# Kernel optimization log

Measured on AMD Instinct MI355X. Metric: run time of the kernel, lower is better.

The kernel has to match this reference:

```python
import jax, jax.numpy as jnp
import numpy as np

D_MODEL = 1024
D_K = 1024
D_V = 1024
N_HEAD = 16
EPS = 1e-5
BS, N_TOK = 2, 2048


def setup_inputs() -> dict:
    key = jax.random.key(0)
    ks = jax.random.split(key, 12)
    s = 0.02
    q = jax.random.normal(ks[0], (BS, N_TOK, D_MODEL), jnp.float32)
    k = jax.random.normal(ks[1], (BS, N_TOK, D_MODEL), jnp.float32)
    v = jax.random.normal(ks[2], (BS, N_TOK, D_MODEL), jnp.float32)
    return {
        "q": q, "k": k, "v": v,
        "gamma": jnp.ones((D_MODEL,), jnp.float32),
        "beta": jnp.zeros((D_MODEL,), jnp.float32),
        "Wq": jax.random.normal(ks[3], (D_MODEL, D_K), jnp.float32) * s,
        "bq": jnp.zeros((D_K,), jnp.float32),
        "Wk": jax.random.normal(ks[4], (D_MODEL, D_K), jnp.float32) * s,
        "bk": jnp.zeros((D_K,), jnp.float32),
        "Wv": jax.random.normal(ks[5], (D_MODEL, D_V), jnp.float32) * s,
        "bv": jnp.zeros((D_V,), jnp.float32),
        "Wo": jax.random.normal(ks[6], (D_V, D_MODEL), jnp.float32) * s,
        "bo": jnp.zeros((D_MODEL,), jnp.float32),
    }


def reference(q, k, v, gamma, beta, Wq, bq, Wk, bk, Wv, bv, Wo, bo):
    # NOTE: original module ignores k, v args; self-attention over q.
    bs, n_tok, d_m = q.shape
    d_h = D_K // N_HEAD
    temper = float(np.sqrt(d_h))

    # LayerNorm1d over d_model
    mu = jnp.mean(q, axis=-1, keepdims=True)
    var = jnp.var(q, axis=-1, keepdims=True)
    h = (q - mu) / jnp.sqrt(var + EPS) * gamma + beta

    # projections; head split = chunk along feature dim -> [bs, H, T, d_h]
    qh = (h @ Wq + bq).reshape(bs, n_tok, N_HEAD, d_h).transpose(0, 2, 1, 3)
    kh = (h @ Wk + bk).reshape(bs, n_tok, N_HEAD, d_h).transpose(0, 2, 1, 3)
    vh = jax.nn.relu(h @ Wv + bv).reshape(bs, n_tok, N_HEAD, d_h).transpose(0, 2, 1, 3)

    scores = jnp.einsum('bhqd,bhkd->bhqk', qh, kh) / temper
    # dropout before softmax in train mode; identity in eval (deterministic ref)
    attn = jax.nn.softmax(scores, axis=-1)
    o = jnp.einsum('bhqk,bhkd->bhqd', attn, vh)  # [bs, H, T, d_h]

    # faithful to torch: view(bs, n_tok, -1) with NO head transpose (head-major merge)
    merged = o.reshape(bs, n_tok, N_HEAD * d_h)
    out = merged @ Wo + bo + q  # proj + residual
    return out
```

## Files before the change

### kernel.cpp

```cpp
#include <hip/hip_runtime.h>

typedef __bf16 bf16;
typedef __bf16 bf16x8 __attribute__((ext_vector_type(8)));
typedef __bf16 bf16x4 __attribute__((ext_vector_type(4)));
typedef float  f32x4  __attribute__((ext_vector_type(4)));
typedef float  f32x16 __attribute__((ext_vector_type(16)));
typedef unsigned int u32;
typedef u32 u32x4 __attribute__((ext_vector_type(4)));

#define AS1U(p) ((const __attribute__((address_space(1))) unsigned int*)(p))
#define AS3U(p) ((__attribute__((address_space(3))) unsigned int*)(p))

static __device__ __forceinline__ u32 pack2(float a, float b) {
    unsigned short ua = __builtin_bit_cast(unsigned short, (bf16)a);
    unsigned short ub = __builtin_bit_cast(unsigned short, (bf16)b);
    return (u32)ua | ((u32)ub << 16);
}

__global__ void transpose_cast4_kernel(const float* __restrict__ W0, const float* __restrict__ W1,
                                       const float* __restrict__ W2, const float* __restrict__ W3,
                                       bf16* __restrict__ D0, bf16* __restrict__ D1,
                                       bf16* __restrict__ D2, bf16* __restrict__ D3) {
    __shared__ float tile[32][33];
    const float* W; bf16* D;
    switch (blockIdx.z) {
        case 0: W = W0; D = D0; break;
        case 1: W = W1; D = D1; break;
        case 2: W = W2; D = D2; break;
        default: W = W3; D = D3; break;
    }
    const int bj = blockIdx.x, bi = blockIdx.y;
    const int tx = threadIdx.x, ty = threadIdx.y;
#pragma unroll
    for (int i = 0; i < 4; i++) {
        tile[ty + i * 8][tx] = W[(size_t)(bi * 32 + ty + i * 8) * 1024 + bj * 32 + tx];
    }
    __syncthreads();
#pragma unroll
    for (int i = 0; i < 4; i++) {
        D[(size_t)(bj * 32 + ty + i * 8) * 1024 + bi * 32 + tx] =
            (bf16)tile[tx][ty + i * 8];
    }
}

__global__ void layernorm_kernel(const float* __restrict__ x,
                                 const float* __restrict__ gamma,
                                 const float* __restrict__ beta,
                                 bf16* __restrict__ h) {
    const int row = blockIdx.x;
    const float* xr = x + (size_t)row * 1024;
    const int t = threadIdx.x;
    float4 v = ((const float4*)xr)[t];
    float s  = v.x + v.y + v.z + v.w;
    float s2 = v.x * v.x + v.y * v.y + v.z * v.z + v.w * v.w;
#pragma unroll
    for (int m = 1; m < 64; m <<= 1) {
        s  += __shfl_xor(s, m, 64);
        s2 += __shfl_xor(s2, m, 64);
    }
    __shared__ float ssum[4], ssum2[4];
    const int wid = t >> 6, lane = t & 63;
    if (lane == 0) { ssum[wid] = s; ssum2[wid] = s2; }
    __syncthreads();
    s  = ssum[0] + ssum[1] + ssum[2] + ssum[3];
    s2 = ssum2[0] + ssum2[1] + ssum2[2] + ssum2[3];
    const float mu  = s * (1.f / 1024.f);
    const float var = s2 * (1.f / 1024.f) - mu * mu;
    const float rs  = rsqrtf(var + 1e-5f);
    float4 g = ((const float4*)gamma)[t];
    float4 b = ((const float4*)beta)[t];
    bf16x4 o;
    o[0] = (bf16)((v.x - mu) * rs * g.x + b.x);
    o[1] = (bf16)((v.y - mu) * rs * g.y + b.y);
    o[2] = (bf16)((v.z - mu) * rs * g.z + b.z);
    o[3] = (bf16)((v.w - mu) * rs * g.w + b.w);
    ((bf16x4*)(h + (size_t)row * 1024))[t] = o;
}

template <int EPI>
__global__ void gemm_kernel(const bf16* __restrict__ A, const bf16* __restrict__ BT,
                            int N, int K,
                            bf16* __restrict__ Cb,
                            const float* __restrict__ b0, const float* __restrict__ b1,
                            const float* __restrict__ b2, bf16* __restrict__ Vt,
                            float* __restrict__ Cf, const float* __restrict__ bo,
                            const float* __restrict__ resid) {
    __shared__ bf16 Asm[128][32];
    __shared__ bf16 Bsm[128][32];
    const int tid = threadIdx.x;
    const int lane = tid & 63, wave = tid >> 6;
    const int wr = wave >> 1, wc = wave & 1;
    const int nwg = gridDim.x * gridDim.y;
    const int bid0 = blockIdx.y * gridDim.x + blockIdx.x;
    const int bid = (bid0 & 7) * (nwg >> 3) + (bid0 >> 3);
    const int tileN = (bid % gridDim.x) * 128;
    const int tileM = (bid / gridDim.x) * 128;
    const int row16 = lane & 15, g = lane >> 4;

    f32x4 acc[4][4] = {};

    for (int kt = 0; kt < K; kt += 32) {
#pragma unroll
        for (int i = 0; i < 2; i++) {
            int c = tid + i * 256;
            int r = c >> 2, cb = (c & 3) * 16;
            const char* g_ = (const char*)(A + (size_t)(tileM + r) * K + kt) + cb;
            char* l_ = (char*)&Asm[0][0] + c * 16;
            __builtin_amdgcn_global_load_lds(AS1U(g_), AS3U(l_), 16, 0, 0);
        }
#pragma unroll
        for (int i = 0; i < 2; i++) {
            int c = tid + i * 256;
            int r = c >> 2, cb = (c & 3) * 16;
            const char* g_ = (const char*)(BT + (size_t)(tileN + r) * K + kt) + cb;
            char* l_ = (char*)&Bsm[0][0] + c * 16;
            __builtin_amdgcn_global_load_lds(AS1U(g_), AS3U(l_), 16, 0, 0);
        }
        __syncthreads();
        bf16x8 af[4], bfr[4];
#pragma unroll
        for (int m = 0; m < 4; m++)
            af[m] = *(const bf16x8*)&Asm[wr * 64 + m * 16 + row16][g * 8];
#pragma unroll
        for (int n = 0; n < 4; n++)
            bfr[n] = *(const bf16x8*)&Bsm[wc * 64 + n * 16 + row16][g * 8];
#pragma unroll
        for (int m = 0; m < 4; m++)
#pragma unroll
            for (int n = 0; n < 4; n++)
                acc[m][n] = __builtin_amdgcn_mfma_f32_16x16x32_bf16(af[m], bfr[n],
                                                                   acc[m][n], 0, 0, 0);
        __syncthreads();
    }

    if constexpr (EPI == 0) {
        __shared__ bf16 Ep[4][64][64];
        char* ep = (char*)&Ep[wave][0][0];
        const bool isV = (tileN >= 2048);
        if (!isV) {
#pragma unroll
            for (int n = 0; n < 4; n++) {
                const int cl = n * 16 + row16;
                const int gc = tileN + wc * 64 + cl;
                const float bias = gc < 1024 ? b0[gc] : b1[gc - 1024];
                const float scl = gc < 1024 ? 0.18033688011112042f : 1.f;
#pragma unroll
                for (int m = 0; m < 4; m++)
#pragma unroll
                    for (int j = 0; j < 4; j++) {
                        const int rl = m * 16 + g * 4 + j;
                        const float v = (acc[m][n][j] + bias) * scl;
                        *(bf16*)(ep + rl * 128 + ((cl * 2) ^ ((rl & 7) << 4))) = (bf16)v;
                    }
            }
        } else {
#pragma unroll
            for (int n = 0; n < 4; n++) {
                const int dl = n * 16 + row16;
                const float bias = b2[(tileN - 2048) + wc * 64 + dl];
#pragma unroll
                for (int m = 0; m < 4; m++)
#pragma unroll
                    for (int j = 0; j < 4; j++) {
                        const int tl = m * 16 + g * 4 + j;
                        const float v = fmaxf(acc[m][n][j] + bias, 0.f);
                        *(bf16*)(ep + dl * 128 + ((tl * 2) ^ ((dl & 7) << 4))) = (bf16)v;
                    }
            }
        }
        asm volatile("s_waitcnt lgkmcnt(0)" ::: "memory");
        __builtin_amdgcn_sched_barrier(0);
        if (!isV) {
#pragma unroll
            for (int it = 0; it < 8; it++) {
                const int rl = (lane >> 3) + it * 8;
                const bf16x8 vrow = *(const bf16x8*)(ep + rl * 128 +
                                                     (((lane & 7) * 16) ^ ((rl & 7) << 4)));
                const int gr = tileM + wr * 64 + rl;
                const int gc = tileN + wc * 64 + (lane & 7) * 8;
                *(bf16x8*)&Cb[(size_t)gr * N + gc] = vrow;
            }
        } else {
            const int bb = tileM >> 11;
            const int tbase = (tileM & 2047) + wr * 64 + (lane & 7) * 8;
#pragma unroll
            for (int it = 0; it < 8; it++) {
                const int dl = (lane >> 3) + it * 8;
                const bf16x8 vrow = *(const bf16x8*)(ep + dl * 128 +
                                                     (((lane & 7) * 16) ^ ((dl & 7) << 4)));
                const int gd = (tileN - 2048) + wc * 64 + dl;
                const int hh = gd >> 6, dd = gd & 63;
                *(bf16x8*)&Vt[(((size_t)bb * 16 + hh) * 64 + dd) * 2048 + tbase] = vrow;
            }
        }
    } else {
#pragma unroll
        for (int m = 0; m < 4; m++) {
            const int row = tileM + wr * 64 + m * 16 + g * 4;
#pragma unroll
            for (int n = 0; n < 4; n++) {
                const int col = tileN + wc * 64 + n * 16 + row16;
#pragma unroll
                for (int j = 0; j < 4; j++) {
                    const int r = row + j;
                    Cf[(size_t)r * N + col] = acc[m][n][j] + bo[col] +
                                              resid[(size_t)r * N + col];
                }
            }
        }
    }
}

__global__ __launch_bounds__(512, 4)
void attn_kernel(const bf16* __restrict__ qkv, const bf16* __restrict__ Vt,
                 bf16* __restrict__ Obuf) {
    const int bid = blockIdx.x;
    const int swz = (bid & 7) * 64 + (bid >> 3);
    const int bh = swz >> 4, qt = swz & 15;
    const int b = bh >> 4, h = bh & 15;
    const int qbase = qt * 128;
    const int tid = threadIdx.x;
    const int lane = tid & 63, wv = tid >> 6;
    const int half = wv >> 2, qw = wv & 3;
    const int c = lane & 31, p = lane >> 5;

    __shared__ bf16 Kl[2][2][64][64];
    __shared__ bf16 Vl[2][2][64][64];

    const bf16* qrow = qkv + (size_t)(b * 2048 + qbase + qw * 32 + c) * 3072 + h * 64;
    bf16x8 qf[4];
#pragma unroll
    for (int ch = 0; ch < 4; ch++)
        qf[ch] = *(const bf16x8*)(qrow + ch * 16 + p * 8);

    const char* kgbase = (const char*)(qkv + (size_t)b * 2048 * 3072 + 1024 + h * 64)
                         + (size_t)(half * 1024) * 6144;
    const char* vgbase = (const char*)(Vt + (size_t)bh * 64 * 2048) + half * 2048;
    const int ht = tid & 255;
    const char* kgp[2]; const char* vgp[2]; int ldo[2];
#pragma unroll
    for (int i = 0; i < 2; i++) {
        const int cc = ht + i * 256;
        const int srow = cc >> 3;
        const int scol = ((cc & 7) * 16) ^ ((srow & 7) << 4);
        kgp[i] = kgbase + (size_t)srow * 6144 + scol;
        vgp[i] = vgbase + (size_t)srow * 4096 + scol;
        ldo[i] = cc * 16;
    }
    char* kldb = (char*)&Kl[half][0][0][0];
    char* vldb = (char*)&Vl[half][0][0][0];

    auto stage = [&](int t, int slot) {
        const size_t ko = (size_t)t * (64 * 6144);
        const size_t vo = (size_t)t * 128;
        const int sb = slot * 8192;
#pragma unroll
        for (int i = 0; i < 2; i++) {
            __builtin_amdgcn_global_load_lds(AS1U(kgp[i] + ko), AS3U(kldb + sb + ldo[i]), 16, 0, 0);
            __builtin_amdgcn_global_load_lds(AS1U(vgp[i] + vo), AS3U(vldb + sb + ldo[i]), 16, 0, 0);
        }
    };

    f32x16 accO[2] = {};
    float l_r = 0.f;

    auto compute = [&](int slot) {
        const char* Kb = (const char*)&Kl[half][slot][0][0];
        const char* Vb = (const char*)&Vl[half][slot][0][0];
#pragma unroll
        for (int cc = 0; cc < 2; cc++) {
            f32x16 accT = {};
            const int tok = cc * 32 + c;
#pragma unroll
            for (int ch = 0; ch < 4; ch++) {
                const bf16x8 kf = *(const bf16x8*)(Kb + tok * 128 +
                                                   ((ch * 32 + p * 16) ^ ((tok & 7) << 4)));
                accT = __builtin_amdgcn_mfma_f32_32x32x16_bf16(kf, qf[ch], accT, 0, 0, 0);
            }
            float pv[16];
#pragma unroll
            for (int r = 0; r < 16; r++) pv[r] = exp2f(accT[r]);
            float s01 = (pv[0] + pv[1]) + (pv[2] + pv[3]);
            float s23 = (pv[4] + pv[5]) + (pv[6] + pv[7]);
            float s45 = (pv[8] + pv[9]) + (pv[10] + pv[11]);
            float s67 = (pv[12] + pv[13]) + (pv[14] + pv[15]);
            l_r += (s01 + s23) + (s45 + s67);
            u32 k01 = pack2(pv[0], pv[1]),  k23 = pack2(pv[2], pv[3]);
            u32 k45 = pack2(pv[4], pv[5]),  k67 = pack2(pv[6], pv[7]);
            u32 k89 = pack2(pv[8], pv[9]),  kab = pack2(pv[10], pv[11]);
            u32 kcd = pack2(pv[12], pv[13]), kef = pack2(pv[14], pv[15]);
            asm("v_permlane32_swap_b32 %0, %1" : "+v"(k45), "+v"(k01));
            asm("v_permlane32_swap_b32 %0, %1" : "+v"(k67), "+v"(k23));
            asm("v_permlane32_swap_b32 %0, %1" : "+v"(kcd), "+v"(k89));
            asm("v_permlane32_swap_b32 %0, %1" : "+v"(kef), "+v"(kab));
            u32x4 w0w = {k01, k23, k45, k67};
            u32x4 w1w = {k89, kab, kcd, kef};
            const bf16x8 pf0 = __builtin_bit_cast(bf16x8, w0w);
            const bf16x8 pf1 = __builtin_bit_cast(bf16x8, w1w);
#pragma unroll
            for (int dc = 0; dc < 2; dc++) {
                const int rd = dc * 32 + c;
                const int sw = (rd & 7) << 4;
                const bf16x8 vf0 = *(const bf16x8*)(Vb + rd * 128 + ((cc * 64 + p * 16) ^ sw));
                const bf16x8 vf1 = *(const bf16x8*)(Vb + rd * 128 + ((cc * 64 + 32 + p * 16) ^ sw));
                accO[dc] = __builtin_amdgcn_mfma_f32_32x32x16_bf16(pf0, vf0, accO[dc], 0, 0, 0);
                accO[dc] = __builtin_amdgcn_mfma_f32_32x32x16_bf16(pf1, vf1, accO[dc], 0, 0, 0);
            }
        }
    };

#define KV_SYNC() do { \
        asm volatile("s_waitcnt vmcnt(0)" ::: "memory"); \
        __builtin_amdgcn_s_barrier(); \
        asm volatile("" ::: "memory"); \
    } while (0)

    stage(0, 0);
#pragma unroll 1
    for (int t = 0; t < 14; t += 2) {
        KV_SYNC(); stage(t + 1, 1); compute(0);
        KV_SYNC(); stage(t + 2, 0); compute(1);
    }
    KV_SYNC(); stage(15, 1); compute(0);
    KV_SYNC(); compute(1);
#undef KV_SYNC

    __syncthreads();
    float* ex = (float*)&Kl[0][0][0][0];
    const int xb = (qw * 64 + lane) * 33;
    if (half) {
#pragma unroll
        for (int dc = 0; dc < 2; dc++)
#pragma unroll
            for (int r = 0; r < 16; r++) ex[xb + dc * 16 + r] = accO[dc][r];
        ex[xb + 32] = l_r;
    }
    __syncthreads();
    if (!half) {
#pragma unroll
        for (int dc = 0; dc < 2; dc++)
#pragma unroll
            for (int r = 0; r < 16; r++) accO[dc][r] += ex[xb + dc * 16 + r];
        l_r += ex[xb + 32];
        l_r += __shfl_xor(l_r, 32);
        const float linv = 1.f / l_r;
        float li[16];
#pragma unroll
        for (int r = 0; r < 16; r++)
            li[r] = __shfl(linv, (r & 3) + 8 * (r >> 2) + 4 * p);
        bf16* ob = Obuf + ((size_t)bh * 2048 + qbase + qw * 32) * 64;
#pragma unroll
        for (int dc = 0; dc < 2; dc++)
#pragma unroll
            for (int r = 0; r < 16; r++) {
                const int row = (r & 3) + 8 * (r >> 2) + 4 * p;
                ob[(size_t)row * 64 + dc * 32 + c] = (bf16)(accO[dc][r] * li[r]);
            }
    }
}

extern "C" void kernel_launch(void* const* d_in, const int* in_sizes, int n_in,
                              void* d_out, int out_size, void* d_ws, size_t ws_size,
                              hipStream_t stream) {
    const float* q     = (const float*)d_in[0];
    const float* gamma = (const float*)d_in[3];
    const float* beta  = (const float*)d_in[4];
    const float* Wq    = (const float*)d_in[5];
    const float* bq    = (const float*)d_in[6];
    const float* Wk    = (const float*)d_in[7];
    const float* bk    = (const float*)d_in[8];
    const float* Wv    = (const float*)d_in[9];
    const float* bv    = (const float*)d_in[10];
    const float* Wo    = (const float*)d_in[11];
    const float* bo    = (const float*)d_in[12];
    float* out = (float*)d_out;

    char* ws = (char*)d_ws;
    bf16* h     = (bf16*)(ws);
    bf16* WcatT = (bf16*)(ws + (8u << 20));
    bf16* WoT   = (bf16*)(ws + (14u << 20));
    bf16* qkv   = (bf16*)(ws + (16u << 20));
    bf16* Obuf  = (bf16*)(ws + (40u << 20));
    bf16* Vtb   = (bf16*)(ws + (48u << 20));

    transpose_cast4_kernel<<<dim3(32, 32, 4), dim3(32, 8), 0, stream>>>(
        Wq, Wk, Wv, Wo,
        WcatT, WcatT + (size_t)1024 * 1024, WcatT + (size_t)2048 * 1024, WoT);

    layernorm_kernel<<<4096, 256, 0, stream>>>(q, gamma, beta, h);

    gemm_kernel<0><<<dim3(24, 32), 256, 0, stream>>>(h, WcatT, 3072, 1024,
                                                     qkv, bq, bk, bv, Vtb,
                                                     nullptr, nullptr, nullptr);

    attn_kernel<<<512, 512, 0, stream>>>(qkv, Vtb, Obuf);

    gemm_kernel<1><<<dim3(8, 32), 256, 0, stream>>>(Obuf, WoT, 1024, 1024,
                                                    nullptr, nullptr, nullptr, nullptr, nullptr,
                                                    out, bo, q);
}
```

Baseline: 131.2 us.

## Fuse prep kernels, stage output-GEMM epilogue in LDS, compute softmax sums via MFMA

Merges the layernorm and weight transpose/cast kernels into one launch, removing a kernel boundary. The output GEMM epilogue now stages bias-added accumulators in shared memory so residual reads and output writes become coalesced float4 accesses. In attention, the softmax row sums are computed with extra MFMAs against a ones vector instead of scalar adds and shuffles. The costs are more LDS use in the GEMM epilogue and two extra MFMAs per tile in attention, which could lower occupancy or lengthen the MFMA pipeline.

```diff
diff --git a/kernel.cpp b/kernel.cpp
--- a/kernel.cpp
+++ b/kernel.cpp
@@ -17,64 +17,66 @@
     return (u32)ua | ((u32)ub << 16);
 }
 
-__global__ void transpose_cast4_kernel(const float* __restrict__ W0, const float* __restrict__ W1,
-                                       const float* __restrict__ W2, const float* __restrict__ W3,
-                                       bf16* __restrict__ D0, bf16* __restrict__ D1,
-                                       bf16* __restrict__ D2, bf16* __restrict__ D3) {
+__global__ void prep_kernel(const float* __restrict__ q,
+                            const float* __restrict__ gamma,
+                            const float* __restrict__ beta,
+                            bf16* __restrict__ h,
+                            const float* __restrict__ W0, const float* __restrict__ W1,
+                            const float* __restrict__ W2, const float* __restrict__ W3,
+                            bf16* __restrict__ D0, bf16* __restrict__ D1,
+                            bf16* __restrict__ D2, bf16* __restrict__ D3) {
     __shared__ float tile[32][33];
-    const float* W; bf16* D;
-    switch (blockIdx.z) {
-        case 0: W = W0; D = D0; break;
-        case 1: W = W1; D = D1; break;
-        case 2: W = W2; D = D2; break;
-        default: W = W3; D = D3; break;
-    }
-    const int bj = blockIdx.x, bi = blockIdx.y;
-    const int tx = threadIdx.x, ty = threadIdx.y;
-#pragma unroll
-    for (int i = 0; i < 4; i++) {
-        tile[ty + i * 8][tx] = W[(size_t)(bi * 32 + ty + i * 8) * 1024 + bj * 32 + tx];
-    }
-    __syncthreads();
-#pragma unroll
-    for (int i = 0; i < 4; i++) {
-        D[(size_t)(bj * 32 + ty + i * 8) * 1024 + bi * 32 + tx] =
-            (bf16)tile[tx][ty + i * 8];
-    }
-}
-
-__global__ void layernorm_kernel(const float* __restrict__ x,
-                                 const float* __restrict__ gamma,
-                                 const float* __restrict__ beta,
-                                 bf16* __restrict__ h) {
-    const int row = blockIdx.x;
-    const float* xr = x + (size_t)row * 1024;
+    __shared__ float ssum[4], ssum2[4];
+    const int blk = blockIdx.x;
     const int t = threadIdx.x;
-    float4 v = ((const float4*)xr)[t];
-    float s  = v.x + v.y + v.z + v.w;
-    float s2 = v.x * v.x + v.y * v.y + v.z * v.z + v.w * v.w;
-#pragma unroll
-    for (int m = 1; m < 64; m <<= 1) {
-        s  += __shfl_xor(s, m, 64);
-        s2 += __shfl_xor(s2, m, 64);
-    }
-    __shared__ float ssum[4], ssum2[4];
-    const int wid = t >> 6, lane = t & 63;
-    if (lane == 0) { ssum[wid] = s; ssum2[wid] = s2; }
-    __syncthreads();
-    s  = ssum[0] + ssum[1] + ssum[2] + ssum[3];
-    s2 = ssum2[0] + ssum2[1] + ssum2[2] + ssum2[3];
-    const float mu  = s * (1.f / 1024.f);
-    const float var = s2 * (1.f / 1024.f) - mu * mu;
-    const float rs  = rsqrtf(var + 1e-5f);
-    float4 g = ((const float4*)gamma)[t];
-    float4 b = ((const float4*)beta)[t];
-    bf16x4 o;
-    o[0] = (bf16)((v.x - mu) * rs * g.x + b.x);
-    o[1] = (bf16)((v.y - mu) * rs * g.y + b.y);
-    o[2] = (bf16)((v.z - mu) * rs * g.z + b.z);
-    o[3] = (bf16)((v.w - mu) * rs * g.w + b.w);
-    ((bf16x4*)(h + (size_t)row * 1024))[t] = o;
+    if (blk < 4096) {
+        const float* xr = q + (size_t)blk * 1024;
+        float4 v = ((const float4*)xr)[t];
+        float s  = v.x + v.y + v.z + v.w;
+        float s2 = v.x * v.x + v.y * v.y + v.z * v.z + v.w * v.w;
+#pragma unroll
+        for (int m = 1; m < 64; m <<= 1) {
+            s  += __shfl_xor(s, m, 64);
+            s2 += __shfl_xor(s2, m, 64);
+        }
+        const int wid = t >> 6, lane = t & 63;
+        if (lane == 0) { ssum[wid] = s; ssum2[wid] = s2; }
+        __syncthreads();
+        s  = ssum[0] + ssum[1] + ssum[2] + ssum[3];
+        s2 = ssum2[0] + ssum2[1] + ssum2[2] + ssum2[3];
+        const float mu  = s * (1.f / 1024.f);
+        const float var = s2 * (1.f / 1024.f) - mu * mu;
+        const float rs  = rsqrtf(var + 1e-5f);
+        float4 g = ((const float4*)gamma)[t];
+        float4 b = ((const float4*)beta)[t];
+        bf16x4 o;
+        o[0] = (bf16)((v.x - mu) * rs * g.x + b.x);
+        o[1] = (bf16)((v.y - mu) * rs * g.y + b.y);
+        o[2] = (bf16)((v.z - mu) * rs * g.z + b.z);
+        o[3] = (bf16)((v.w - mu) * rs * g.w + b.w);
+        ((bf16x4*)(h + (size_t)blk * 1024))[t] = o;
+    } else {
+        const int z = blk - 4096;
+        const float* W; bf16* D;
+        switch (z >> 10) {
+            case 0: W = W0; D = D0; break;
+            case 1: W = W1; D = D1; break;
+            case 2: W = W2; D = D2; break;
+            default: W = W3; D = D3; break;
+        }
+        const int bi = (z & 1023) >> 5, bj = z & 31;
+        const int tx = t & 31, ty = t >> 5;
+#pragma unroll
+        for (int i = 0; i < 4; i++) {
+            tile[ty + i * 8][tx] = W[(size_t)(bi * 32 + ty + i * 8) * 1024 + bj * 32 + tx];
+        }
+        __syncthreads();
+#pragma unroll
+        for (int i = 0; i < 4; i++) {
+            D[(size_t)(bj * 32 + ty + i * 8) * 1024 + bi * 32 + tx] =
+                (bf16)tile[tx][ty + i * 8];
+        }
+    }
 }
 
 template <int EPI>
@@ -194,19 +196,33 @@
             }
         }
     } else {
-#pragma unroll
-        for (int m = 0; m < 4; m++) {
-            const int row = tileM + wr * 64 + m * 16 + g * 4;
-#pragma unroll
-            for (int n = 0; n < 4; n++) {
-                const int col = tileN + wc * 64 + n * 16 + row16;
+        __shared__ float Epf[4][64][66];
+        float* ep = &Epf[wave][0][0];
+#pragma unroll
+        for (int n = 0; n < 4; n++) {
+            const int cl = n * 16 + row16;
+            const float bias = bo[tileN + wc * 64 + cl];
+#pragma unroll
+            for (int m = 0; m < 4; m++)
 #pragma unroll
                 for (int j = 0; j < 4; j++) {
-                    const int r = row + j;
-                    Cf[(size_t)r * N + col] = acc[m][n][j] + bo[col] +
-                                              resid[(size_t)r * N + col];
+                    const int rl = m * 16 + g * 4 + j;
+                    ep[rl * 66 + cl] = acc[m][n][j] + bias;
                 }
-            }
+        }
+        asm volatile("s_waitcnt lgkmcnt(0)" ::: "memory");
+        __builtin_amdgcn_sched_barrier(0);
+        const int rl0 = lane >> 4;
+        const int cl0 = (lane & 15) * 4;
+#pragma unroll
+        for (int it = 0; it < 16; it++) {
+            const int rl = rl0 + it * 4;
+            float4 v = *(const float4*)&ep[rl * 66 + cl0];
+            const int gr = tileM + wr * 64 + rl;
+            const int gc = tileN + wc * 64 + cl0;
+            const float4 rv = *(const float4*)&resid[(size_t)gr * N + gc];
+            v.x += rv.x; v.y += rv.y; v.z += rv.z; v.w += rv.w;
+            *(float4*)&Cf[(size_t)gr * N + gc] = v;
         }
     }
 }
@@ -262,17 +278,22 @@
     };
 
     f32x16 accO[2] = {};
-    float l_r = 0.f;
+    f32x16 accL = {};
+    const f32x16 z16 = {};
+    const u32 one2 = 0x3F803F80u;
+    const u32x4 onesw = {one2, one2, one2, one2};
+    const bf16x8 onesf = __builtin_bit_cast(bf16x8, onesw);
 
     auto compute = [&](int slot) {
         const char* Kb = (const char*)&Kl[half][slot][0][0];
         const char* Vb = (const char*)&Vl[half][slot][0][0];
 #pragma unroll
         for (int cc = 0; cc < 2; cc++) {
-            f32x16 accT = {};
             const int tok = cc * 32 + c;
-#pragma unroll
-            for (int ch = 0; ch < 4; ch++) {
+            const bf16x8 kf0 = *(const bf16x8*)(Kb + tok * 128 + ((0 * 32 + p * 16) ^ ((tok & 7) << 4)));
+            f32x16 accT = __builtin_amdgcn_mfma_f32_32x32x16_bf16(kf0, qf[0], z16, 0, 0, 0);
+#pragma unroll
+            for (int ch = 1; ch < 4; ch++) {
                 const bf16x8 kf = *(const bf16x8*)(Kb + tok * 128 +
                                                    ((ch * 32 + p * 16) ^ ((tok & 7) << 4)));
                 accT = __builtin_amdgcn_mfma_f32_32x32x16_bf16(kf, qf[ch], accT, 0, 0, 0);
@@ -280,11 +301,6 @@
             float pv[16];
 #pragma unroll
             for (int r = 0; r < 16; r++) pv[r] = exp2f(accT[r]);
-            float s01 = (pv[0] + pv[1]) + (pv[2] + pv[3]);
-            float s23 = (pv[4] + pv[5]) + (pv[6] + pv[7]);
-            float s45 = (pv[8] + pv[9]) + (pv[10] + pv[11]);
-            float s67 = (pv[12] + pv[13]) + (pv[14] + pv[15]);
-            l_r += (s01 + s23) + (s45 + s67);
             u32 k01 = pack2(pv[0], pv[1]),  k23 = pack2(pv[2], pv[3]);
             u32 k45 = pack2(pv[4], pv[5]),  k67 = pack2(pv[6], pv[7]);
             u32 k89 = pack2(pv[8], pv[9]),  kab = pack2(pv[10], pv[11]);
@@ -297,6 +313,8 @@
             u32x4 w1w = {k89, kab, kcd, kef};
             const bf16x8 pf0 = __builtin_bit_cast(bf16x8, w0w);
             const bf16x8 pf1 = __builtin_bit_cast(bf16x8, w1w);
+            accL = __builtin_amdgcn_mfma_f32_32x32x16_bf16(pf0, onesf, accL, 0, 0, 0);
+            accL = __builtin_amdgcn_mfma_f32_32x32x16_bf16(pf1, onesf, accL, 0, 0, 0);
 #pragma unroll
             for (int dc = 0; dc < 2; dc++) {
                 const int rd = dc * 32 + c;
@@ -327,13 +345,14 @@
 
     __syncthreads();
     float* ex = (float*)&Kl[0][0][0][0];
-    const int xb = (qw * 64 + lane) * 33;
+    const int xb = (qw * 64 + lane) * 49;
     if (half) {
 #pragma unroll
         for (int dc = 0; dc < 2; dc++)
 #pragma unroll
             for (int r = 0; r < 16; r++) ex[xb + dc * 16 + r] = accO[dc][r];
-        ex[xb + 32] = l_r;
+#pragma unroll
+        for (int r = 0; r < 16; r++) ex[xb + 32 + r] = accL[r];
     }
     __syncthreads();
     if (!half) {
@@ -341,21 +360,16 @@
         for (int dc = 0; dc < 2; dc++)
 #pragma unroll
             for (int r = 0; r < 16; r++) accO[dc][r] += ex[xb + dc * 16 + r];
-        l_r += ex[xb + 32];
-        l_r += __shfl_xor(l_r, 32);
-        const float linv = 1.f / l_r;
-        float li[16];
-#pragma unroll
-        for (int r = 0; r < 16; r++)
-            li[r] = __shfl(linv, (r & 3) + 8 * (r >> 2) + 4 * p);
+#pragma unroll
+        for (int r = 0; r < 16; r++) accL[r] += ex[xb + 32 + r];
         bf16* ob = Obuf + ((size_t)bh * 2048 + qbase + qw * 32) * 64;
 #pragma unroll
-        for (int dc = 0; dc < 2; dc++)
-#pragma unroll
-            for (int r = 0; r < 16; r++) {
-                const int row = (r & 3) + 8 * (r >> 2) + 4 * p;
-                ob[(size_t)row * 64 + dc * 32 + c] = (bf16)(accO[dc][r] * li[r]);
-            }
+        for (int r = 0; r < 16; r++) {
+            const float inv = 1.f / accL[r];
+            const int row = (r & 3) + 8 * (r >> 2) + 4 * p;
+            ob[(size_t)row * 64 + c]      = (bf16)(accO[0][r] * inv);
+            ob[(size_t)row * 64 + 32 + c] = (bf16)(accO[1][r] * inv);
+        }
     }
 }
 
@@ -383,11 +397,10 @@
     bf16* Obuf  = (bf16*)(ws + (40u << 20));
     bf16* Vtb   = (bf16*)(ws + (48u << 20));
 
-    transpose_cast4_kernel<<<dim3(32, 32, 4), dim3(32, 8), 0, stream>>>(
-        Wq, Wk, Wv, Wo,
-        WcatT, WcatT + (size_t)1024 * 1024, WcatT + (size_t)2048 * 1024, WoT);
-
-    layernorm_kernel<<<4096, 256, 0, stream>>>(q, gamma, beta, h);
+    prep_kernel<<<8192, 256, 0, stream>>>(q, gamma, beta, h,
+                                          Wq, Wk, Wv, Wo,
+                                          WcatT, WcatT + (size_t)1024 * 1024,
+                                          WcatT + (size_t)2048 * 1024, WoT);
 
     gemm_kernel<0><<<dim3(24, 32), 256, 0, stream>>>(h, WcatT, 3072, 1024,
                                                      qkv, bq, bk, bv, Vtb,
```

Measured after the change: 128.1 us. 1.02x faster.
